# Kernel optimization log

Measured on AMD Instinct MI355X. Metric: run time of the kernel, lower is better.

Reference implementation:

```python
import jax, jax.numpy as jnp
import numpy as np

NUM_HEADS = 8  # from init_kwargs


def setup_inputs() -> dict:
    key = jax.random.key(0)
    ks = jax.random.split(key, 8)
    B, N, Din, H, Dout, E = 4, 2048, 256, 512, 256, 65536
    s = 0.02
    return {
        "x": jax.random.normal(ks[0], (B, N, Din), jnp.float32),
        "edge_index": jax.random.randint(ks[1], (2, E), 0, N),
        "W_gcn": jax.random.normal(ks[2], (Din, H), jnp.float32) * s,
        "b_gcn": jnp.zeros((H,), jnp.float32),
        "in_proj_w": jax.random.normal(ks[3], (3 * H, H), jnp.float32) * s,
        "in_proj_b": jnp.zeros((3 * H,), jnp.float32),
        "out_proj_w": jax.random.normal(ks[4], (H, H), jnp.float32) * s,
        "out_proj_b": jnp.zeros((H,), jnp.float32),
        "fc_w": jax.random.normal(ks[5], (H, Dout), jnp.float32) * s,
        "fc_b": jnp.zeros((Dout,), jnp.float32),
    }


def _gcn(x, edge_index, W, b):
    # PyG GCNConv: add self-loops, symmetric normalization, gather-scatter aggregation.
    B, N, _ = x.shape
    loop = jnp.arange(N)
    src = jnp.concatenate([edge_index[0], loop])  # message source j
    dst = jnp.concatenate([edge_index[1], loop])  # aggregation target i
    deg = jnp.zeros((N,), x.dtype).at[dst].add(1.0)
    dinv = jnp.where(deg > 0, jax.lax.rsqrt(deg), 0.0)
    norm = dinv[src] * dinv[dst]                  # [Etot]
    xl = x @ W                                    # [B, N, H]
    msgs = xl[:, src, :] * norm[None, :, None]    # [B, Etot, H]
    out = jnp.zeros_like(xl).at[:, dst].add(msgs)  # scatter-add over edges
    return out + b


def _mha(x_nbh, wi, bi, wo, bo, nh):
    # torch MultiheadAttention, input [N(seq), B, H], self-attention.
    N, B, H = x_nbh.shape
    dh = H // nh
    qkv = x_nbh @ wi.T + bi                       # [N, B, 3H]
    q, k, v = jnp.split(qkv, 3, axis=-1)
    q = q.reshape(N, B, nh, dh) * (dh ** -0.5)
    k = k.reshape(N, B, nh, dh)
    v = v.reshape(N, B, nh, dh)
    scores = jnp.einsum("nbhd,mbhd->bhnm", q, k)  # [B, nh, N, N]
    attn = jax.nn.softmax(scores, axis=-1)
    o = jnp.einsum("bhnm,mbhd->nbhd", attn, v).reshape(N, B, H)
    return o @ wo.T + bo


def reference(x, edge_index, W_gcn, b_gcn, in_proj_w, in_proj_b,
              out_proj_w, out_proj_b, fc_w, fc_b):
    h = _gcn(x, edge_index, W_gcn, b_gcn)         # [B, N, H]
    h = jnp.transpose(h, (1, 0, 2))               # [N, B, H]
    h = _mha(h, in_proj_w, in_proj_b, out_proj_w, out_proj_b, NUM_HEADS)
    h = jnp.transpose(h, (1, 0, 2))               # [B, N, H]
    h = jax.nn.relu(h)
    return h @ fc_w + fc_b                        # [B, N, Dout]
```

## Files before the change

### kernel.cpp

```cpp
#include <hip/hip_runtime.h>
#include <hip/hip_bf16.h>


#define NN 2048
#define HH 512
#define NHEAD 8
#define DH 64

typedef _Float16 f16;
typedef __attribute__((ext_vector_type(2))) _Float16 f16x2;
typedef __attribute__((ext_vector_type(4))) _Float16 f16x4;
typedef __attribute__((ext_vector_type(8))) _Float16 f16x8;
typedef __attribute__((ext_vector_type(4))) float f32x4;

#define GLOAD_LDS16(g, l)                                              \
  __builtin_amdgcn_global_load_lds(                                    \
      (const __attribute__((address_space(1))) void*)(g),              \
      (__attribute__((address_space(3))) void*)(l), 16, 0, 0)

__device__ __forceinline__ float fast_exp2(float x) {
#if __has_builtin(__builtin_amdgcn_exp2f)
  return __builtin_amdgcn_exp2f(x);
#else
  return exp2f(x);
#endif
}

__device__ __forceinline__ f16x2 cvt_pk_f16(float a, float b) {
#if __has_builtin(__builtin_amdgcn_cvt_pkrtz)
  return __builtin_bit_cast(f16x2, __builtin_amdgcn_cvt_pkrtz(a, b));
#else
  f16x2 r = { (f16)a, (f16)b };
  return r;
#endif
}


__global__ __launch_bounds__(256) void prep_all_kernel(const float* __restrict__ wi,
                                                       const float* __restrict__ wo,
                                                       const float* __restrict__ wg,
                                                       const float* __restrict__ fcw,
                                                       f16* __restrict__ wi16,
                                                       f16* __restrict__ wo16,
                                                       f16* __restrict__ wg16t,
                                                       f16* __restrict__ fcw16t,
                                                       float* __restrict__ deg,
                                                       int* __restrict__ cursor) {
  __shared__ float tbuf[32][33];
  const int bid = blockIdx.x, t = threadIdx.x;
  if (bid < 768) {
    const int i = bid * 256 + t;
    const float4 v = ((const float4*)wi)[i];
    f16x4 o = { (f16)v.x, (f16)v.y, (f16)v.z, (f16)v.w };
    ((f16x4*)wi16)[i] = o;
  } else if (bid < 1024) {
    const int i = (bid - 768) * 256 + t;
    const float4 v = ((const float4*)wo)[i];
    f16x4 o = { (f16)v.x, (f16)v.y, (f16)v.z, (f16)v.w };
    ((f16x4*)wo16)[i] = o;
  } else if (bid == 1024) {
    for (int i = t; i < NN; i += 256) { deg[i] = 0.0f; cursor[i] = 0; }
  } else {
    const int id = bid - 1025;
    const float* in;
    f16* outp;
    int R, C, bx, by;
    if (id < 128) { in = wg;  outp = wg16t;  R = 256; C = 512;
                    bx = id & 15; by = id >> 4; }
    else { int id2 = id - 128; in = fcw; outp = fcw16t; R = 512; C = 256;
           bx = id2 & 7; by = id2 >> 3; }
    const int c0 = bx * 32, r0 = by * 32;
    const int tx = t & 31, ty = t >> 5;
#pragma unroll
    for (int i = 0; i < 32; i += 8) tbuf[ty + i][tx] = in[(size_t)(r0 + ty + i) * C + c0 + tx];
    __syncthreads();
#pragma unroll
    for (int i = 0; i < 32; i += 8)
      outp[(size_t)(c0 + ty + i) * R + r0 + tx] = (f16)tbuf[tx][ty + i];
  }
}


__global__ __launch_bounds__(256) void count_deg_kernel(const int* __restrict__ ei, int E,
                                                        float* __restrict__ deg) {
  int e = blockIdx.x * 256 + threadIdx.x;
  if (e < E) atomicAdd(&deg[ei[E + e]], 1.0f);
}

__global__ __launch_bounds__(1024) void build_rowptr_kernel(const float* __restrict__ deg,
                                                            float* __restrict__ dinv,
                                                            int* __restrict__ rowptr) {
  __shared__ int a[NN];
  __shared__ int bbuf[NN];
  const int t = threadIdx.x;
  for (int i = t; i < NN; i += 1024) {
    float dg = deg[i];
    a[i] = (int)dg;
    dinv[i] = rsqrtf(dg + 1.0f);
  }
  __syncthreads();
  int* src = a;
  int* dst = bbuf;
  for (int off = 1; off < NN; off <<= 1) {
    for (int i = t; i < NN; i += 1024) {
      int v = src[i];
      if (i >= off) v += src[i - off];
      dst[i] = v;
    }
    __syncthreads();
    int* tmp = src; src = dst; dst = tmp;
  }
  for (int i = t; i < NN; i += 1024) rowptr[i + 1] = src[i];
  if (t == 0) rowptr[0] = 0;
}

__global__ __launch_bounds__(256) void fill_csr_kernel(const int* __restrict__ ei, int E,
                                                       const int* __restrict__ rowptr,
                                                       int* __restrict__ cursor,
                                                       int* __restrict__ csr_src) {
  int e = blockIdx.x * 256 + threadIdx.x;
  if (e < E) {
    int s = ei[e];
    int d = ei[E + e];
    int pos = atomicAdd(&cursor[d], 1);
    csr_src[rowptr[d] + pos] = s;
  }
}


template <int OUTMODE, bool BIAS, bool RELU, bool AF32, int MT = 128>
__global__ __launch_bounds__(256) void mfma_gemm_kernel(
    const void* __restrict__ Ap, const f16* __restrict__ Bt,
    const float* __restrict__ bias, void* __restrict__ Cout,
    int M, int N, int K,
    f16* __restrict__ q_out, f16* __restrict__ k_out, f16* __restrict__ v_out) {
  constexpr int MI = MT / 32;
  __shared__ f16 As[MT * 32];
  __shared__ f16 Bs[128 * 32];
  const int tid = threadIdx.x;
  const int wave = tid >> 6, lane = tid & 63;
  const int quad = lane >> 4, l16 = lane & 15;
  const int m0 = blockIdx.y * MT, n0 = blockIdx.x * 128;
  const int moff = (wave >> 1) * (MI * 16), noff = (wave & 1) * 64;

  f32x4 acc[MI][4];
#pragma unroll
  for (int i = 0; i < MI; ++i)
#pragma unroll
    for (int j = 0; j < 4; ++j) acc[i][j] = (f32x4){0.f, 0.f, 0.f, 0.f};

  const int rpw = MT / 4;
  const int srowA = rpw * wave + (lane >> 2);
  const int srowB = 32 * wave + (lane >> 2);
  const int kch = (lane & 3) * 8;
  const f16* Ag = (const f16*)Ap + (size_t)(m0 + srowA) * K + kch;
  const float* Ag32 = (const float*)Ap + (size_t)(m0 + srowA) * K + kch;
  const f16* Bg = Bt + (size_t)(n0 + srowB) * K + kch;
  f16* As_w = &As[(rpw * wave) * 32];
  f16* Bs_w = &Bs[(32 * wave) * 32];

  for (int k0 = 0; k0 < K; k0 += 32) {
    __syncthreads();
    if (AF32) {
#pragma unroll
      for (int t = 0; t < 2; ++t) {
        const float* g = Ag32 + k0 + (size_t)(16 * t) * K;
        const float4 u0 = *(const float4*)g;
        const float4 u1 = *(const float4*)(g + 4);
        f16x8 o = { (f16)u0.x, (f16)u0.y, (f16)u0.z, (f16)u0.w,
                    (f16)u1.x, (f16)u1.y, (f16)u1.z, (f16)u1.w };
        *(f16x8*)&As[(srowA + 16 * t) * 32 + kch] = o;
      }
    } else {
      GLOAD_LDS16(Ag + k0, As_w);
      if (MT == 128) GLOAD_LDS16(Ag + k0 + (size_t)16 * K, As_w + 16 * 32);
    }
    GLOAD_LDS16(Bg + k0, Bs_w);
    GLOAD_LDS16(Bg + k0 + (size_t)16 * K, Bs_w + 16 * 32);
    __syncthreads();
    f16x8 af[MI], bf[4];
#pragma unroll
    for (int m16 = 0; m16 < MI; ++m16)
      af[m16] = *(const f16x8*)&As[(moff + m16 * 16 + l16) * 32 + quad * 8];
#pragma unroll
    for (int n16 = 0; n16 < 4; ++n16)
      bf[n16] = *(const f16x8*)&Bs[(noff + n16 * 16 + l16) * 32 + quad * 8];
#pragma unroll
    for (int m16 = 0; m16 < MI; ++m16)
#pragma unroll
      for (int n16 = 0; n16 < 4; ++n16)
        acc[m16][n16] =
            __builtin_amdgcn_mfma_f32_16x16x32_f16(af[m16], bf[n16], acc[m16][n16], 0, 0, 0);
  }

  float bv[4];
#pragma unroll
  for (int n16 = 0; n16 < 4; ++n16)
    bv[n16] = BIAS ? bias[n0 + noff + n16 * 16 + l16] : 0.f;

  if (OUTMODE == 2) {
    const int hblk = (n0 >> 6) + (wave & 1);
    const int which = hblk >> 3, h = hblk & 7;
    f16* dst = (which == 0) ? q_out : (which == 1) ? k_out : v_out;
    const float scale = (which == 0) ? 0.125f * 1.44269504088896340736f : 1.0f;
#pragma unroll
    for (int m16 = 0; m16 < MI; ++m16) {
#pragma unroll
      for (int r = 0; r < 4; ++r) {
        const int m = m0 + moff + m16 * 16 + quad * 4 + r;
        const int b = m >> 11, ns = m & 2047;
        f16* row = dst + ((size_t)(b * 8 + h) * NN + ns) * DH;
#pragma unroll
        for (int n16 = 0; n16 < 4; ++n16) {
          const int d = n16 * 16 + l16;
          row[d] = (f16)((acc[m16][n16][r] + bv[n16]) * scale);
        }
      }
    }
  } else {
#pragma unroll
    for (int m16 = 0; m16 < MI; ++m16) {
#pragma unroll
      for (int r = 0; r < 4; ++r) {
        const size_t row = (size_t)(m0 + moff + m16 * 16 + quad * 4 + r) * N;
#pragma unroll
        for (int n16 = 0; n16 < 4; ++n16) {
          const int col = n0 + noff + n16 * 16 + l16;
          float v = acc[m16][n16][r] + bv[n16];
          if (RELU) v = fmaxf(v, 0.f);
          if (OUTMODE == 0) ((float*)Cout)[row + col] = v;
          else ((f16*)Cout)[row + col] = (f16)v;
        }
      }
    }
  }
}


__global__ __launch_bounds__(256) void gcn_aggregate_kernel(const f16* __restrict__ xl,
                                                            const float* __restrict__ dinv,
                                                            const int* __restrict__ rowptr,
                                                            const int* __restrict__ csr_src,
                                                            const float* __restrict__ b_gcn,
                                                            f16* __restrict__ out) {
  __shared__ int s_src[256];
  __shared__ float s_dv[256];
  const int i = blockIdx.x;
  const int tid = threadIdx.x;
  const float dv_i = dinv[i];
  const int b = tid >> 6;
  const int f = (tid & 63) * 8;
  const f16* xb = xl + (size_t)(b * NN) * HH + f;
  float acc[8];
  {
    const f16x8 self = *(const f16x8*)&xb[(size_t)i * HH];
#pragma unroll
    for (int j = 0; j < 8; ++j) acc[j] = (float)self[j] * dv_i;
  }
  const int beg = rowptr[i], end = rowptr[i + 1];
  for (int c0 = beg; c0 < end; c0 += 256) {
    const int cnt = min(256, end - c0);
    __syncthreads();
    if (tid < cnt) {
      int s = csr_src[c0 + tid];
      s_src[tid] = s;
      s_dv[tid] = dinv[s];
    }
    __syncthreads();
    for (int t = 0; t < cnt; ++t) {
      const f16x8 v = *(const f16x8*)&xb[(size_t)s_src[t] * HH];
      const float w = s_dv[t];
#pragma unroll
      for (int j = 0; j < 8; ++j) acc[j] = fmaf((float)v[j], w, acc[j]);
    }
  }
  const float4 bg0 = *(const float4*)&b_gcn[f];
  const float4 bg1 = *(const float4*)&b_gcn[f + 4];
  f16x8 o;
  o[0] = (f16)(acc[0] * dv_i + bg0.x);
  o[1] = (f16)(acc[1] * dv_i + bg0.y);
  o[2] = (f16)(acc[2] * dv_i + bg0.z);
  o[3] = (f16)(acc[3] * dv_i + bg0.w);
  o[4] = (f16)(acc[4] * dv_i + bg1.x);
  o[5] = (f16)(acc[5] * dv_i + bg1.y);
  o[6] = (f16)(acc[6] * dv_i + bg1.z);
  o[7] = (f16)(acc[7] * dv_i + bg1.w);
  *(f16x8*)&out[((size_t)(b * NN) + i) * HH + f] = o;
}


__global__ __launch_bounds__(256, 2) void flash_attn_f16_kernel(const f16* __restrict__ Qb,
                                                                const f16* __restrict__ Kb,
                                                                const f16* __restrict__ Vb,
                                                                f16* __restrict__ out) {
  constexpr int LDK = 72;
  constexpr int LDV = 128;
  __shared__ f16 Ks[128 * LDK];
  __shared__ f16 Vt[64 * LDV];
  const int tid = threadIdx.x;
  const int wave = tid >> 6, lane = tid & 63;
  const int quad = lane >> 4, l16 = lane & 15;
  const int bid = blockIdx.x;
  const int sw = (bid & 7) * 64 + (bid >> 3);
  const int bh = sw >> 4;
  const int n0 = (sw & 15) * 128;
  const int b = bh >> 3, h = bh & 7;
  const f16* kb = Kb + (size_t)bh * NN * DH;
  const f16* vb = Vb + (size_t)bh * NN * DH;

  f16x8 aq[2][2];
#pragma unroll
  for (int g = 0; g < 2; ++g) {
    const f16* qf = Qb + ((size_t)bh * NN + n0 + (wave + 4 * g) * 16 + l16) * DH + quad * 8;
    aq[g][0] = *(const f16x8*)qf;
    aq[g][1] = *(const f16x8*)(qf + 32);
  }

  float l_part[2] = {0.f, 0.f};
  f32x4 acc_o[2][4];
#pragma unroll
  for (int g = 0; g < 2; ++g)
#pragma unroll
    for (int n16 = 0; n16 < 4; ++n16) acc_o[g][n16] = (f32x4){0.f, 0.f, 0.f, 0.f};

  const int kr = tid >> 3, kc = (tid & 7) * 8;
  const int vdg = tid & 15, jbb = tid >> 4;
  int fdr[4];
#pragma unroll
  for (int n16 = 0; n16 < 4; ++n16)
    fdr[n16] = (2 * n16 + l16 + (l16 >> 3)) & 7;

  f16x8 kreg[4];
  f16x4 vreg[2][4];

  auto load_tile = [&](int k0) {
#pragma unroll
    for (int i = 0; i < 4; ++i)
      kreg[i] = *(const f16x8*)(kb + (size_t)(k0 + kr + 32 * i) * DH + kc);
#pragma unroll
    for (int cc = 0; cc < 2; ++cc) {
      const int jb = jbb + 16 * cc;
#pragma unroll
      for (int i = 0; i < 4; ++i)
        vreg[cc][i] = *(const f16x4*)(vb + (size_t)(k0 + jb * 4 + i) * DH + vdg * 4);
    }
  };
  auto store_tile = [&]() {
#pragma unroll
    for (int i = 0; i < 4; ++i)
      *(f16x8*)&Ks[(kr + 32 * i) * LDK + kc] = kreg[i];
#pragma unroll
    for (int cc = 0; cc < 2; ++cc) {
      const int jb = jbb + 16 * cc;
      const int vch = (jb >> 3) * 4 + (jb & 3);
      const int vrem = ((jb >> 2) & 1) * 4;
#pragma unroll
      for (int c = 0; c < 4; ++c) {
        const int d = vdg * 4 + c;
        const int fd = (d + (d >> 3)) & 7;
        const int off = (((vch & 8) | ((vch ^ fd) & 7)) << 3) + vrem;
        f16x4 o = { vreg[cc][0][c], vreg[cc][1][c], vreg[cc][2][c], vreg[cc][3][c] };
        *(f16x4*)&Vt[d * LDV + off] = o;
      }
    }
  };
  auto do_p = [&](int p) {
    f32x4 sA[2][2];
#pragma unroll
    for (int t = 0; t < 2; ++t) {
      const f16x8 ak0 = *(const f16x8*)&Ks[(p * 32 + t * 16 + l16) * LDK + quad * 8];
      const f16x8 ak1 = *(const f16x8*)&Ks[(p * 32 + t * 16 + l16) * LDK + quad * 8 + 32];
#pragma unroll
      for (int g = 0; g < 2; ++g) {
        f32x4 s = {0.f, 0.f, 0.f, 0.f};
        s = __builtin_amdgcn_mfma_f32_16x16x32_f16(ak0, aq[g][0], s, 0, 0, 0);
        s = __builtin_amdgcn_mfma_f32_16x16x32_f16(ak1, aq[g][1], s, 0, 0, 0);
        sA[g][t] = s;
      }
    }
    f16x8 bvv[4];
    const int chp = p * 4 + quad;
#pragma unroll
    for (int n16 = 0; n16 < 4; ++n16) {
      const int off = ((chp & 8) | ((chp ^ fdr[n16]) & 7)) << 3;
      bvv[n16] = *(const f16x8*)&Vt[(n16 * 16 + l16) * LDV + off];
    }
#pragma unroll
    for (int g = 0; g < 2; ++g) {
      union { f16x8 v; f16x2 hh[4]; } ap;
      float sum = 0.f;
#pragma unroll
      for (int t = 0; t < 2; ++t)
#pragma unroll
        for (int rr = 0; rr < 2; ++rr) {
          const float e0 = fast_exp2(sA[g][t][rr * 2]);
          const float e1 = fast_exp2(sA[g][t][rr * 2 + 1]);
          sum += e0 + e1;
          ap.hh[t * 2 + rr] = cvt_pk_f16(e0, e1);
        }
      l_part[g] += sum;
#pragma unroll
      for (int n16 = 0; n16 < 4; ++n16)
        acc_o[g][n16] = __builtin_amdgcn_mfma_f32_16x16x32_f16(ap.v, bvv[n16], acc_o[g][n16], 0, 0, 0);
    }
  };

  load_tile(0);
  store_tile();
  __syncthreads();
  for (int kt = 0; kt < NN / 128; ++kt) {
    const bool pf = (kt + 1) < (NN / 128);
    if (pf) load_tile((kt + 1) * 128);
    __builtin_amdgcn_s_setprio(1);
    do_p(0);
    do_p(1);
    do_p(2);
    do_p(3);
    __builtin_amdgcn_s_setprio(0);
    __syncthreads();
    if (pf) {
      store_tile();
      __syncthreads();
    }
  }

#pragma unroll
  for (int g = 0; g < 2; ++g) {
    float lp = l_part[g];
    lp += __shfl_xor(lp, 16);
    lp += __shfl_xor(lp, 32);
    f16* obase = out + ((size_t)b * NN + n0 + (wave + 4 * g) * 16) * HH + h * DH;
#pragma unroll
    for (int r = 0; r < 4; ++r) {
      const float lr = __shfl(lp, (lane & 48) | (quad * 4 + r));
      const float inv = 1.0f / lr;
#pragma unroll
      for (int n16 = 0; n16 < 4; ++n16)
        obase[(size_t)(quad * 4 + r) * HH + n16 * 16 + l16] = (f16)(acc_o[g][n16][r] * inv);
    }
  }
}


extern "C" void kernel_launch(void* const* d_in, const int* in_sizes, int n_in,
                              void* d_out, int out_size, void* d_ws, size_t ws_size,
                              hipStream_t stream) {
  const float* x     = (const float*)d_in[0];
  const int*   ei    = (const int*)d_in[1];
  const float* W_gcn = (const float*)d_in[2];
  const float* b_gcn = (const float*)d_in[3];
  const float* wi    = (const float*)d_in[4];
  const float* bi    = (const float*)d_in[5];
  const float* wo    = (const float*)d_in[6];
  const float* bo    = (const float*)d_in[7];
  const float* fcw   = (const float*)d_in[8];
  const float* fcb   = (const float*)d_in[9];
  float* out = (float*)d_out;
  const int E = in_sizes[1] / 2;
  const int M = 4 * NN;

  char* wsb = (char*)d_ws;
  const size_t MB = 1u << 20;
  f16* xl16   = (f16*)(wsb + 4 * MB);
  f16* hb16   = (f16*)(wsb + 12 * MB);
  f16* Qb     = (f16*)(wsb + 20 * MB);
  f16* Kb     = (f16*)(wsb + 28 * MB);
  f16* Vb     = (f16*)(wsb + 36 * MB);
  f16* attn16 = (f16*)(wsb + 44 * MB);
  f16* proj16 = (f16*)(wsb + 52 * MB);
  f16* wi16   = (f16*)(wsb + 60 * MB);
  f16* wo16   = (f16*)(wsb + 62 * MB);
  f16* wg16t  = (f16*)(wsb + 63 * MB);
  f16* fcw16t = (f16*)(wsb + 64 * MB);
  float* deg  = (float*)(wsb + 65 * MB);
  float* dinv = deg + NN;
  int* rowptr = (int*)(dinv + NN);
  int* cursor = rowptr + 2080;
  int* csr    = cursor + NN;

  prep_all_kernel<<<1281, 256, 0, stream>>>(wi, wo, W_gcn, fcw, wi16, wo16,
                                            wg16t, fcw16t, deg, cursor);

  count_deg_kernel<<<(E + 255) / 256, 256, 0, stream>>>(ei, E, deg);
  build_rowptr_kernel<<<1, 1024, 0, stream>>>(deg, dinv, rowptr);
  fill_csr_kernel<<<(E + 255) / 256, 256, 0, stream>>>(ei, E, rowptr, cursor, csr);

  mfma_gemm_kernel<1, false, false, true><<<dim3(4, 64), 256, 0, stream>>>(
      x, wg16t, nullptr, xl16, M, 512, 256, nullptr, nullptr, nullptr);
  gcn_aggregate_kernel<<<NN, 256, 0, stream>>>(xl16, dinv, rowptr, csr, b_gcn, hb16);
  mfma_gemm_kernel<2, true, false, false><<<dim3(12, 64), 256, 0, stream>>>(
      hb16, wi16, bi, nullptr, M, 1536, 512, Qb, Kb, Vb);
  flash_attn_f16_kernel<<<512, 256, 0, stream>>>(Qb, Kb, Vb, attn16);
  mfma_gemm_kernel<1, true, true, false><<<dim3(4, 64), 256, 0, stream>>>(
      attn16, wo16, bo, proj16, M, 512, 512, nullptr, nullptr, nullptr);
  mfma_gemm_kernel<0, true, false, false, 64><<<dim3(2, 128), 256, 0, stream>>>(
      proj16, fcw16t, fcb, out, M, 256, 512, nullptr, nullptr, nullptr);
}
```

Baseline: 234.7 us.

## Split attention over key halves with atomic fp32 partials, normalize in out-proj

```diff
diff --git a/kernel.cpp b/kernel.cpp
--- a/kernel.cpp
+++ b/kernel.cpp
@@ -128,12 +128,13 @@
 }
 
 
-template <int OUTMODE, bool BIAS, bool RELU, bool AF32, int MT = 128>
+template <int OUTMODE, bool BIAS, bool RELU, bool AF32, int MT = 128, bool ANORM = false>
 __global__ __launch_bounds__(256) void mfma_gemm_kernel(
     const void* __restrict__ Ap, const f16* __restrict__ Bt,
     const float* __restrict__ bias, void* __restrict__ Cout,
     int M, int N, int K,
-    f16* __restrict__ q_out, f16* __restrict__ k_out, f16* __restrict__ v_out) {
+    f16* __restrict__ q_out, f16* __restrict__ k_out, f16* __restrict__ v_out,
+    const float* __restrict__ l_norm) {
   constexpr int MI = MT / 32;
   __shared__ f16 As[MT * 32];
   __shared__ f16 Bs[128 * 32];
@@ -161,14 +162,21 @@
 
   for (int k0 = 0; k0 < K; k0 += 32) {
     __syncthreads();
-    if (AF32) {
+    if (AF32 || ANORM) {
 #pragma unroll
       for (int t = 0; t < 2; ++t) {
         const float* g = Ag32 + k0 + (size_t)(16 * t) * K;
         const float4 u0 = *(const float4*)g;
         const float4 u1 = *(const float4*)(g + 4);
-        f16x8 o = { (f16)u0.x, (f16)u0.y, (f16)u0.z, (f16)u0.w,
-                    (f16)u1.x, (f16)u1.y, (f16)u1.z, (f16)u1.w };
+        float sc = 1.0f;
+        if (ANORM) {
+          const int m = m0 + srowA + 16 * t;
+          const int bb = m >> 11, nn = m & 2047;
+          const int hh = k0 >> 6;
+          sc = 1.0f / l_norm[(size_t)(bb * 8 + hh) * NN + nn];
+        }
+        f16x8 o = { (f16)(u0.x * sc), (f16)(u0.y * sc), (f16)(u0.z * sc), (f16)(u0.w * sc),
+                    (f16)(u1.x * sc), (f16)(u1.y * sc), (f16)(u1.z * sc), (f16)(u1.w * sc) };
         *(f16x8*)&As[(srowA + 16 * t) * 32 + kch] = o;
       }
     } else {
@@ -289,10 +297,11 @@
 }
 
 
-__global__ __launch_bounds__(256, 2) void flash_attn_f16_kernel(const f16* __restrict__ Qb,
+__global__ __launch_bounds__(256, 4) void flash_attn_f16_kernel(const f16* __restrict__ Qb,
                                                                 const f16* __restrict__ Kb,
                                                                 const f16* __restrict__ Vb,
-                                                                f16* __restrict__ out) {
+                                                                float* __restrict__ Op,
+                                                                float* __restrict__ Lp) {
   constexpr int LDK = 72;
   constexpr int LDV = 128;
   __shared__ f16 Ks[128 * LDK];
@@ -301,10 +310,13 @@
   const int wave = tid >> 6, lane = tid & 63;
   const int quad = lane >> 4, l16 = lane & 15;
   const int bid = blockIdx.x;
-  const int sw = (bid & 7) * 64 + (bid >> 3);
-  const int bh = sw >> 4;
-  const int n0 = (sw & 15) * 128;
+  const int sw = (bid & 7) * 128 + (bid >> 3);
+  const int bh = sw >> 5;
+  const int qt = (sw >> 1) & 15;
+  const int half = sw & 1;
+  const int n0 = qt * 128;
   const int b = bh >> 3, h = bh & 7;
+  const int kbase = half * (NN / 2);
   const f16* kb = Kb + (size_t)bh * NN * DH;
   const f16* vb = Vb + (size_t)bh * NN * DH;
 
@@ -405,12 +417,12 @@
     }
   };
 
-  load_tile(0);
+  load_tile(kbase);
   store_tile();
   __syncthreads();
-  for (int kt = 0; kt < NN / 128; ++kt) {
-    const bool pf = (kt + 1) < (NN / 128);
-    if (pf) load_tile((kt + 1) * 128);
+  for (int kt = 0; kt < 8; ++kt) {
+    const bool pf = (kt + 1) < 8;
+    if (pf) load_tile(kbase + (kt + 1) * 128);
     __builtin_amdgcn_s_setprio(1);
     do_p(0);
     do_p(1);
@@ -429,15 +441,15 @@
     float lp = l_part[g];
     lp += __shfl_xor(lp, 16);
     lp += __shfl_xor(lp, 32);
-    f16* obase = out + ((size_t)b * NN + n0 + (wave + 4 * g) * 16) * HH + h * DH;
-#pragma unroll
-    for (int r = 0; r < 4; ++r) {
-      const float lr = __shfl(lp, (lane & 48) | (quad * 4 + r));
-      const float inv = 1.0f / lr;
+    const int qrow0 = n0 + (wave + 4 * g) * 16;
+    if (quad == 0)
+      atomicAdd(&Lp[(size_t)bh * NN + qrow0 + l16], lp);
+    float* obase = Op + ((size_t)b * NN + qrow0) * HH + h * DH;
+#pragma unroll
+    for (int r = 0; r < 4; ++r)
 #pragma unroll
       for (int n16 = 0; n16 < 4; ++n16)
-        obase[(size_t)(quad * 4 + r) * HH + n16 * 16 + l16] = (f16)(acc_o[g][n16][r] * inv);
-    }
+        atomicAdd(&obase[(size_t)(quad * 4 + r) * HH + n16 * 16 + l16], acc_o[g][n16][r]);
   }
 }
 
@@ -461,12 +473,13 @@
 
   char* wsb = (char*)d_ws;
   const size_t MB = 1u << 20;
+  float* Opart = (float*)(wsb + 0);
+  float* Lpart = (float*)(wsb + 16 * MB);
   f16* xl16   = (f16*)(wsb + 4 * MB);
   f16* hb16   = (f16*)(wsb + 12 * MB);
   f16* Qb     = (f16*)(wsb + 20 * MB);
   f16* Kb     = (f16*)(wsb + 28 * MB);
   f16* Vb     = (f16*)(wsb + 36 * MB);
-  f16* attn16 = (f16*)(wsb + 44 * MB);
   f16* proj16 = (f16*)(wsb + 52 * MB);
   f16* wi16   = (f16*)(wsb + 60 * MB);
   f16* wo16   = (f16*)(wsb + 62 * MB);
@@ -486,13 +499,14 @@
   fill_csr_kernel<<<(E + 255) / 256, 256, 0, stream>>>(ei, E, rowptr, cursor, csr);
 
   mfma_gemm_kernel<1, false, false, true><<<dim3(4, 64), 256, 0, stream>>>(
-      x, wg16t, nullptr, xl16, M, 512, 256, nullptr, nullptr, nullptr);
+      x, wg16t, nullptr, xl16, M, 512, 256, nullptr, nullptr, nullptr, nullptr);
   gcn_aggregate_kernel<<<NN, 256, 0, stream>>>(xl16, dinv, rowptr, csr, b_gcn, hb16);
   mfma_gemm_kernel<2, true, false, false><<<dim3(12, 64), 256, 0, stream>>>(
-      hb16, wi16, bi, nullptr, M, 1536, 512, Qb, Kb, Vb);
-  flash_attn_f16_kernel<<<512, 256, 0, stream>>>(Qb, Kb, Vb, attn16);
-  mfma_gemm_kernel<1, true, true, false><<<dim3(4, 64), 256, 0, stream>>>(
-      attn16, wo16, bo, proj16, M, 512, 512, nullptr, nullptr, nullptr);
+      hb16, wi16, bi, nullptr, M, 1536, 512, Qb, Kb, Vb, nullptr);
+  hipMemsetAsync(wsb, 0, 16 * MB + 262144, stream);
+  flash_attn_f16_kernel<<<1024, 256, 0, stream>>>(Qb, Kb, Vb, Opart, Lpart);
+  mfma_gemm_kernel<1, true, true, false, 128, true><<<dim3(4, 64), 256, 0, stream>>>(
+      Opart, wo16, bo, proj16, M, 512, 512, nullptr, nullptr, nullptr, Lpart);
   mfma_gemm_kernel<0, true, false, false, 64><<<dim3(2, 128), 256, 0, stream>>>(
-      proj16, fcw16t, fcb, out, M, 256, 512, nullptr, nullptr, nullptr);
-}
+      proj16, fcw16t, fcb, out, M, 256, 512, nullptr, nullptr, nullptr, nullptr);
+}
```

After: 357.9 us. +52.5%, slower.

## Split flash attention key range across two wave groups and merge via LDS

Applied to the files above, without the earlier changes.

```diff
diff --git a/kernel.cpp b/kernel.cpp
--- a/kernel.cpp
+++ b/kernel.cpp
@@ -289,29 +289,35 @@
 }
 
 
-__global__ __launch_bounds__(256, 2) void flash_attn_f16_kernel(const f16* __restrict__ Qb,
+__global__ __launch_bounds__(512, 4) void flash_attn_f16_kernel(const f16* __restrict__ Qb,
                                                                 const f16* __restrict__ Kb,
                                                                 const f16* __restrict__ Vb,
                                                                 f16* __restrict__ out) {
   constexpr int LDK = 72;
   constexpr int LDV = 128;
-  __shared__ f16 Ks[128 * LDK];
-  __shared__ f16 Vt[64 * LDV];
+  __shared__ __align__(16) char smem_raw[69632];
   const int tid = threadIdx.x;
   const int wave = tid >> 6, lane = tid & 63;
   const int quad = lane >> 4, l16 = lane & 15;
+  const int w4 = wave & 3, half = wave >> 2;
   const int bid = blockIdx.x;
   const int sw = (bid & 7) * 64 + (bid >> 3);
   const int bh = sw >> 4;
   const int n0 = (sw & 15) * 128;
   const int b = bh >> 3, h = bh & 7;
+  const int kbase = half * (NN / 2);
   const f16* kb = Kb + (size_t)bh * NN * DH;
   const f16* vb = Vb + (size_t)bh * NN * DH;
 
+  f16* Ks = (f16*)smem_raw + half * (128 * LDK);
+  f16* Vt = (f16*)(smem_raw + 2 * 128 * LDK * 2) + half * (64 * LDV);
+  float* cb = (float*)smem_raw;
+  float* l_lds = (float*)(smem_raw + 33792);
+
   f16x8 aq[2][2];
 #pragma unroll
   for (int g = 0; g < 2; ++g) {
-    const f16* qf = Qb + ((size_t)bh * NN + n0 + (wave + 4 * g) * 16 + l16) * DH + quad * 8;
+    const f16* qf = Qb + ((size_t)bh * NN + n0 + (w4 + 4 * g) * 16 + l16) * DH + quad * 8;
     aq[g][0] = *(const f16x8*)qf;
     aq[g][1] = *(const f16x8*)(qf + 32);
   }
@@ -323,8 +329,9 @@
 #pragma unroll
     for (int n16 = 0; n16 < 4; ++n16) acc_o[g][n16] = (f32x4){0.f, 0.f, 0.f, 0.f};
 
-  const int kr = tid >> 3, kc = (tid & 7) * 8;
-  const int vdg = tid & 15, jbb = tid >> 4;
+  const int t256 = tid & 255;
+  const int kr = t256 >> 3, kc = (t256 & 7) * 8;
+  const int vdg = t256 & 15, jbb = t256 >> 4;
   int fdr[4];
 #pragma unroll
   for (int n16 = 0; n16 < 4; ++n16)
@@ -405,12 +412,12 @@
     }
   };
 
-  load_tile(0);
+  load_tile(kbase);
   store_tile();
   __syncthreads();
-  for (int kt = 0; kt < NN / 128; ++kt) {
-    const bool pf = (kt + 1) < (NN / 128);
-    if (pf) load_tile((kt + 1) * 128);
+  for (int kt = 0; kt < 8; ++kt) {
+    const bool pf = (kt + 1) < 8;
+    if (pf) load_tile(kbase + (kt + 1) * 128);
     __builtin_amdgcn_s_setprio(1);
     do_p(0);
     do_p(1);
@@ -424,19 +431,44 @@
     }
   }
 
+  float lt[2];
 #pragma unroll
   for (int g = 0; g < 2; ++g) {
     float lp = l_part[g];
     lp += __shfl_xor(lp, 16);
     lp += __shfl_xor(lp, 32);
-    f16* obase = out + ((size_t)b * NN + n0 + (wave + 4 * g) * 16) * HH + h * DH;
-#pragma unroll
-    for (int r = 0; r < 4; ++r) {
-      const float lr = __shfl(lp, (lane & 48) | (quad * 4 + r));
-      const float inv = 1.0f / lr;
+    lt[g] = lp;
+  }
+  if (half == 1) {
+#pragma unroll
+    for (int g = 0; g < 2; ++g) {
+      const int row0 = (w4 + 4 * g) * 16 + quad * 4;
 #pragma unroll
       for (int n16 = 0; n16 < 4; ++n16)
-        obase[(size_t)(quad * 4 + r) * HH + n16 * 16 + l16] = (f16)(acc_o[g][n16][r] * inv);
+        *(f32x4*)&cb[(n16 * 16 + l16) * 132 + row0] = acc_o[g][n16];
+      if (quad == 0) l_lds[(w4 + 4 * g) * 16 + l16] = lt[g];
+    }
+  }
+  __syncthreads();
+  if (half == 0) {
+#pragma unroll
+    for (int g = 0; g < 2; ++g) {
+      const float ltot = lt[g] + l_lds[(w4 + 4 * g) * 16 + l16];
+      const int row0 = (w4 + 4 * g) * 16 + quad * 4;
+#pragma unroll
+      for (int n16 = 0; n16 < 4; ++n16) {
+        const f32x4 oh = *(const f32x4*)&cb[(n16 * 16 + l16) * 132 + row0];
+        acc_o[g][n16] += oh;
+      }
+      f16* obase = out + ((size_t)b * NN + n0 + (w4 + 4 * g) * 16) * HH + h * DH;
+#pragma unroll
+      for (int r = 0; r < 4; ++r) {
+        const float lr = __shfl(ltot, (lane & 48) | (quad * 4 + r));
+        const float inv = 1.0f / lr;
+#pragma unroll
+        for (int n16 = 0; n16 < 4; ++n16)
+          obase[(size_t)(quad * 4 + r) * HH + n16 * 16 + l16] = (f16)(acc_o[g][n16][r] * inv);
+      }
     }
   }
 }
@@ -490,7 +522,7 @@
   gcn_aggregate_kernel<<<NN, 256, 0, stream>>>(xl16, dinv, rowptr, csr, b_gcn, hb16);
   mfma_gemm_kernel<2, true, false, false><<<dim3(12, 64), 256, 0, stream>>>(
       hb16, wi16, bi, nullptr, M, 1536, 512, Qb, Kb, Vb);
-  flash_attn_f16_kernel<<<512, 256, 0, stream>>>(Qb, Kb, Vb, attn16);
+  flash_attn_f16_kernel<<<512, 512, 0, stream>>>(Qb, Kb, Vb, attn16);
   mfma_gemm_kernel<1, true, true, false><<<dim3(4, 64), 256, 0, stream>>>(
       attn16, wo16, bo, proj16, M, 512, 512, nullptr, nullptr, nullptr);
   mfma_gemm_kernel<0, true, false, false, 64><<<dim3(2, 128), 256, 0, stream>>>(
```

Result: slower. 362.8 us (+54.6%).
